# Performance work log

Hardware: AMD Instinct MI355X
Metric: run time of the kernel (lower is better)

The kernel has to match this reference:

```python
import jax, jax.numpy as jnp
import numpy as np

N = 2048      # number of ROIs
C = 1024      # in_channels == inter_channels
G = 16        # groups
D = C // G    # per-group dim = 64


def _bbox_overlaps(b1, b2):
    # mmdet-1.x IoU with +1 pixel convention; b1:(N,4), b2:(M,4)
    area1 = (b1[:, 2] - b1[:, 0] + 1) * (b1[:, 3] - b1[:, 1] + 1)  # (N,)
    area2 = (b2[:, 2] - b2[:, 0] + 1) * (b2[:, 3] - b2[:, 1] + 1)  # (M,)
    lt = jnp.maximum(b1[:, None, :2], b2[None, :, :2])             # (N,M,2)
    rb = jnp.minimum(b1[:, None, 2:], b2[None, :, 2:])             # (N,M,2)
    wh = jnp.clip(rb - lt + 1, 0)
    inter = wh[..., 0] * wh[..., 1]                                # (N,M)
    return inter / (area1[:, None] + area2[None, :] - inter)


def setup_inputs() -> dict:
    key = jax.random.key(0)
    ks = jax.random.split(key, 9)
    in_x = jax.random.normal(ks[0], (N, C), dtype=jnp.float32)
    # valid boxes: [batch_idx, x1, y1, x2, y2]
    xy = jax.random.uniform(ks[1], (N, 2), minval=0.0, maxval=800.0)
    wh = jax.random.uniform(ks[2], (N, 2), minval=8.0, maxval=200.0)
    rois = jnp.concatenate([jnp.zeros((N, 1)), xy, xy + wh], axis=1).astype(jnp.float32)
    s = 1.0 / np.sqrt(C)
    W0 = jax.random.normal(ks[3], (C, C), dtype=jnp.float32) * s
    b0 = jnp.zeros((C,), dtype=jnp.float32)
    W1 = jax.random.normal(ks[4], (C, C), dtype=jnp.float32) * s
    b1 = jnp.zeros((C,), dtype=jnp.float32)
    # grouped 1x1 conv: per group maps C channels -> D channels
    Wout = jax.random.normal(ks[5], (G, D, C), dtype=jnp.float32) * s
    bout = jnp.zeros((C,), dtype=jnp.float32)
    return {"in_x": in_x, "rois": rois, "W0": W0, "b0": b0, "W1": W1,
            "b1": b1, "Wout": Wout, "bout": bout}


def reference(in_x, rois, W0, b0, W1, b1, Wout, bout):
    # self-attention path: in_ref_x = in_x, ref_rois = rois
    # embed convs are pre-activation (relu -> 1x1 conv), shared for x and ref_x
    def embed(v):
        v = jax.nn.relu(v) @ W0.T + b0
        v = jax.nn.relu(v) @ W1.T + b1
        return v
    x = embed(in_x)                      # (N, C)
    ref_x = x                            # shared convs, same input
    xg = x.reshape(N, G, D)
    rg = ref_x.reshape(N, G, D)
    scores = jnp.einsum('ngd,mgd->ngm', xg, rg) / jnp.sqrt(jnp.float32(D))  # (N,G,N)
    ious = _bbox_overlaps(rois[:, 1:], rois[:, 1:])                          # (N,N)
    scores = scores + jnp.log(ious[:, None, :] + 1e-6)
    attn = jax.nn.softmax(scores, axis=2)                                    # (N,G,N)
    y = jnp.einsum('ngm,mc->ngc', attn, in_x)                                # (N,G,C)
    out = jnp.einsum('ngc,goc->ngo', y, Wout).reshape(N, C) + bout           # (N,C)
    return out
```

## Files before the change

### kernel.cpp

```cpp
#include <hip/hip_runtime.h>
#include <math.h>

constexpr int NROI = 2048;
constexpr int CDIM = 1024;
constexpr int NG   = 16;
constexpr int DH   = 64;

typedef __attribute__((ext_vector_type(8))) short short8;
typedef __attribute__((ext_vector_type(4))) float floatx4;

#define MFMA_BF16(a, b, c) __builtin_amdgcn_mfma_f32_16x16x32_bf16((a), (b), (c), 0, 0, 0)

__device__ __forceinline__ short f2bf(float f) {
  unsigned u = __float_as_uint(f);
  unsigned r = 0x7fffu + ((u >> 16) & 1u);
  return (short)((u + r) >> 16);
}
__device__ __forceinline__ float bf2f(unsigned short u) {
  return __uint_as_float(((unsigned)u) << 16);
}
__device__ __forceinline__ unsigned pack2(float a, float b) {
  return (unsigned)(unsigned short)f2bf(a) | ((unsigned)(unsigned short)f2bf(b) << 16);
}

typedef __attribute__((address_space(1))) void GV;
typedef __attribute__((address_space(3))) void LV;
__device__ __forceinline__ void gl2lds16(const void* g, void* l) {
  __builtin_amdgcn_global_load_lds((GV*)g, (LV*)l, 16, 0, 0);
}

__device__ __forceinline__ short8 brelu(short8 v) {
  union { short8 s; unsigned u[4]; } x; x.s = v;
#pragma unroll
  for (int i = 0; i < 4; ++i) {
    unsigned m = (x.u[i] >> 15) & 0x10001u;
    x.u[i] &= ~(m * 0xFFFFu);
  }
  return x.s;
}

__global__ __launch_bounds__(256) void convert_kernel(
    const float* __restrict__ in_x, const float* __restrict__ W0,
    const float* __restrict__ W1, const float* __restrict__ Wout,
    short* __restrict__ xin_b, short* __restrict__ W0b,
    short* __restrict__ W1b, short* __restrict__ Woutb)
{
  const int i = blockIdx.x * 256 + threadIdx.x;
  {
    const float4 v = ((const float4*)in_x)[i];
    uint2 u; u.x = pack2(v.x, v.y); u.y = pack2(v.z, v.w);
    ((uint2*)xin_b)[i] = u;
  }
  if (i < 262144) {
    float4 v = ((const float4*)W0)[i];
    uint2 u; u.x = pack2(v.x, v.y); u.y = pack2(v.z, v.w);
    ((uint2*)W0b)[i] = u;
    v = ((const float4*)W1)[i];
    u.x = pack2(v.x, v.y); u.y = pack2(v.z, v.w);
    ((uint2*)W1b)[i] = u;
    v = ((const float4*)Wout)[i];
    u.x = pack2(v.x, v.y); u.y = pack2(v.z, v.w);
    ((uint2*)Woutb)[i] = u;
  }
}

__global__ __launch_bounds__(256) void iou4_kernel(const float* __restrict__ rois,
                                                   unsigned short* __restrict__ biasb)
{
  const int q  = blockIdx.y;
  const int k0 = (blockIdx.x * 256 + threadIdx.x) * 4;
  const float qx1 = rois[q * 5 + 1], qy1 = rois[q * 5 + 2];
  const float qx2 = rois[q * 5 + 3], qy2 = rois[q * 5 + 4];
  const float qa = (qx2 - qx1 + 1.f) * (qy2 - qy1 + 1.f);
  float v[4];
#pragma unroll
  for (int j = 0; j < 4; ++j) {
    const int k = k0 + j;
    const float kx1 = rois[k * 5 + 1], ky1 = rois[k * 5 + 2];
    const float kx2 = rois[k * 5 + 3], ky2 = rois[k * 5 + 4];
    const float ka = (kx2 - kx1 + 1.f) * (ky2 - ky1 + 1.f);
    float iw = fminf(qx2, kx2) - fmaxf(qx1, kx1) + 1.f;
    float ih = fminf(qy2, ky2) - fmaxf(qy1, ky1) + 1.f;
    iw = fmaxf(iw, 0.f); ih = fmaxf(ih, 0.f);
    const float inter = iw * ih;
    v[j] = inter * __builtin_amdgcn_rcpf(qa + ka - inter) + 1e-6f;
  }
  uint2 u; u.x = pack2(v[0], v[1]); u.y = pack2(v[2], v[3]);
  *(uint2*)&biasb[(size_t)q * NROI + k0] = u;
}

template <int FUSED>
__global__ __launch_bounds__(256, 4) void gemm64(
    const short* __restrict__ A, const short* __restrict__ Ba,
    const short* __restrict__ Bb, const float* __restrict__ bias,
    short* __restrict__ outRM, short* __restrict__ outTR)
{
  __shared__ short As[2][8 * 512];
  __shared__ short Bs[2][8 * 512];
  const int t = threadIdx.x, w = t >> 6, lane = t & 63;
  const int wm = w >> 1, wn = w & 1;
  const int row0 = blockIdx.y * 64;
  bool isW0; int col0; const short* B;
  if (FUSED) {
    isW0 = blockIdx.x < 16;
    col0 = (blockIdx.x & 15) * 64;
    B = isW0 ? Ba : Bb;
  } else {
    isW0 = true; col0 = blockIdx.x * 64; B = Ba;
  }
  const bool doRelu = FUSED ? isW0 : true;
  const int rlo = lane & 15, khi = (lane >> 4) * 8;

  floatx4 acc[2][2];
#pragma unroll
  for (int i = 0; i < 2; ++i)
#pragma unroll
    for (int j = 0; j < 2; ++j) acc[i][j] = (floatx4){0.f, 0.f, 0.f, 0.f};

#pragma unroll
  for (int kh = 0; kh < 2; ++kh) {
    const int f = w * 2 + kh;
    gl2lds16(A + (size_t)(row0 + w * 16 + rlo) * CDIM + kh * 32 + khi, &As[0][f * 512]);
    gl2lds16(B + (size_t)(col0 + w * 16 + rlo) * CDIM + kh * 32 + khi, &Bs[0][f * 512]);
  }
  __syncthreads();

  for (int it = 0; it < 16; ++it) {
    const int p = it & 1;
    if (it < 15) {
      const int k1 = (it + 1) * 64;
#pragma unroll
      for (int kh = 0; kh < 2; ++kh) {
        const int f = w * 2 + kh;
        gl2lds16(A + (size_t)(row0 + w * 16 + rlo) * CDIM + k1 + kh * 32 + khi,
                 &As[1 - p][f * 512]);
        gl2lds16(B + (size_t)(col0 + w * 16 + rlo) * CDIM + k1 + kh * 32 + khi,
                 &Bs[1 - p][f * 512]);
      }
    }
#pragma unroll
    for (int kh = 0; kh < 2; ++kh) {
      short8 a[2], bf[2];
#pragma unroll
      for (int i = 0; i < 2; ++i) {
        a[i] = *(const short8*)&As[p][((wm * 2 + i) * 2 + kh) * 512 + lane * 8];
        if (doRelu) a[i] = brelu(a[i]);
      }
#pragma unroll
      for (int j = 0; j < 2; ++j)
        bf[j] = *(const short8*)&Bs[p][((wn * 2 + j) * 2 + kh) * 512 + lane * 8];
#pragma unroll
      for (int i = 0; i < 2; ++i)
#pragma unroll
        for (int j = 0; j < 2; ++j)
          acc[i][j] = MFMA_BF16(a[i], bf[j], acc[i][j]);
    }
    __syncthreads();
  }

  const int colL = lane & 15, qq = lane >> 4;
  if (!FUSED || isW0) {
    float bj[2];
    bj[0] = bias[col0 + wn * 32 + colL];
    bj[1] = bias[col0 + wn * 32 + 16 + colL];
#pragma unroll
    for (int i = 0; i < 2; ++i)
#pragma unroll
      for (int j = 0; j < 2; ++j)
#pragma unroll
        for (int r = 0; r < 4; ++r) {
          const int row = row0 + wm * 32 + i * 16 + qq * 4 + r;
          const int cc  = col0 + wn * 32 + j * 16 + colL;
          outRM[(size_t)row * CDIM + cc] = f2bf(acc[i][j][r] + bj[j]);
        }
  } else {
#pragma unroll
    for (int i = 0; i < 2; ++i)
#pragma unroll
      for (int j = 0; j < 2; ++j) {
        unsigned long long u =
            (unsigned long long)pack2(acc[i][j][0], acc[i][j][1]) |
            ((unsigned long long)pack2(acc[i][j][2], acc[i][j][3]) << 32);
        const int cc  = col0 + wn * 32 + j * 16 + colL;
        const int row = row0 + wm * 32 + i * 16 + qq * 4;
        *(unsigned long long*)&outTR[(size_t)cc * NROI + row] = u;
      }
  }
}

__global__ __launch_bounds__(512) void attn_bias(
    const short* __restrict__ Xb,
    const short* __restrict__ ZTb,
    const unsigned short* __restrict__ biasb,
    const float* __restrict__ bout,
    float* __restrict__ Out)
{
  const int g  = blockIdx.y;
  const int n0 = blockIdx.x * 128;
  const int t  = threadIdx.x;
  const int w    = t >> 6;
  const int lane = t & 63;
  const int col  = lane & 15;
  const int qq   = lane >> 4;
  const int t16 = (w >> 1) * 16;
  const int h32 = (w & 1) * 32;
  const int rlo = lane & 15, khi = (lane >> 4) * 8;

  __shared__ short Kf[2][8 * 512];
  __shared__ short Vf[2][8 * 512];
  __shared__ short Pf[8 * 1024];

  const size_t qoff = (size_t)(n0 + w * 16 + col) * CDIM + g * DH;
  const short8 qf0 = *(const short8*)(Xb + qoff + qq * 8);
  const short8 qf1 = *(const short8*)(Xb + qoff + 32 + qq * 8);

  floatx4 oc[4];
#pragma unroll
  for (int dt = 0; dt < 4; ++dt) oc[dt] = (floatx4){0.f, 0.f, 0.f, 0.f};
  float lsum[4] = {0.f, 0.f, 0.f, 0.f};

  gl2lds16(Xb + (size_t)(t16 + rlo) * CDIM + g * DH + h32 + khi, &Kf[0][w * 512]);
  gl2lds16(ZTb + (size_t)(g * DH + t16 + rlo) * NROI + h32 + khi, &Vf[0][w * 512]);
  __syncthreads();

  for (int it = 0; it < NROI / 64; ++it) {
    const int p  = it & 1;
    const int m0 = it * 64;
    if (it + 1 < NROI / 64) {
      const int m1 = m0 + 64;
      gl2lds16(Xb + (size_t)(m1 + t16 + rlo) * CDIM + g * DH + h32 + khi,
               &Kf[1 - p][w * 512]);
      gl2lds16(ZTb + (size_t)(g * DH + t16 + rlo) * NROI + m1 + h32 + khi,
               &Vf[1 - p][w * 512]);
    }

    float bb[4][4];
#pragma unroll
    for (int ct = 0; ct < 4; ++ct)
#pragma unroll
      for (int r = 0; r < 4; ++r)
        bb[ct][r] = bf2f(biasb[(size_t)(n0 + w * 16 + qq * 4 + r) * NROI +
                               m0 + ct * 16 + col]);

    floatx4 sc[4];
#pragma unroll
    for (int ct = 0; ct < 4; ++ct) {
      const short8 b0 = *(const short8*)&Kf[p][(ct * 2 + 0) * 512 + lane * 8];
      const short8 b1 = *(const short8*)&Kf[p][(ct * 2 + 1) * 512 + lane * 8];
      floatx4 z4 = (floatx4){0.f, 0.f, 0.f, 0.f};
      z4 = MFMA_BF16(qf0, b0, z4);
      z4 = MFMA_BF16(qf1, b1, z4);
      sc[ct] = z4;
    }

#pragma unroll
    for (int ct = 0; ct < 4; ++ct)
#pragma unroll
      for (int r = 0; r < 4; ++r)
        sc[ct][r] = __expf(sc[ct][r] * 0.125f) * bb[ct][r];
#pragma unroll
    for (int r = 0; r < 4; ++r)
      lsum[r] += sc[0][r] + sc[1][r] + sc[2][r] + sc[3][r];

    {
      short* pw = &Pf[w * 1024];
#pragma unroll
      for (int ct = 0; ct < 4; ++ct) {
        const int key = ct * 16 + col;
        const int base = (key >> 5) * 512 + (key & 7);
#pragma unroll
        for (int r = 0; r < 4; ++r) {
          const int dl = (4 * qq + r) + ((key >> 3) & 3) * 16;
          pw[base + dl * 8] = f2bf(sc[ct][r]);
        }
      }
      const short8 pa0 = *(const short8*)&pw[0 * 512 + lane * 8];
      const short8 pa1 = *(const short8*)&pw[1 * 512 + lane * 8];
#pragma unroll
      for (int dt = 0; dt < 4; ++dt) {
        const short8 v0 = *(const short8*)&Vf[p][(dt * 2 + 0) * 512 + lane * 8];
        const short8 v1 = *(const short8*)&Vf[p][(dt * 2 + 1) * 512 + lane * 8];
        oc[dt] = MFMA_BF16(pa0, v0, oc[dt]);
        oc[dt] = MFMA_BF16(pa1, v1, oc[dt]);
      }
    }
    __syncthreads();
  }

#pragma unroll
  for (int r = 0; r < 4; ++r) {
    float s = lsum[r];
    s += __shfl_xor(s, 1); s += __shfl_xor(s, 2);
    s += __shfl_xor(s, 4); s += __shfl_xor(s, 8);
    lsum[r] = s;
  }
#pragma unroll
  for (int dt = 0; dt < 4; ++dt) {
    const float bo = bout[g * DH + dt * 16 + col];
#pragma unroll
    for (int r = 0; r < 4; ++r)
      Out[(size_t)(n0 + w * 16 + qq * 4 + r) * CDIM + g * DH + dt * 16 + col] =
          oc[dt][r] / lsum[r] + bo;
  }
}

extern "C" void kernel_launch(void* const* d_in, const int* in_sizes, int n_in,
                              void* d_out, int out_size, void* d_ws, size_t ws_size,
                              hipStream_t stream) {
  const float* in_x = (const float*)d_in[0];
  const float* rois = (const float*)d_in[1];
  const float* W0   = (const float*)d_in[2];
  const float* b0   = (const float*)d_in[3];
  const float* W1   = (const float*)d_in[4];
  const float* b1   = (const float*)d_in[5];
  const float* Wout = (const float*)d_in[6];
  const float* bout = (const float*)d_in[7];
  char* w8 = (char*)d_ws;

  short* xin_b = (short*)w8;
  short* W0b   = (short*)(w8 + ((size_t)4 << 20));
  short* W1b   = (short*)(w8 + ((size_t)6 << 20));
  short* Woutb = (short*)(w8 + ((size_t)8 << 20));
  short* zT    = (short*)(w8 + ((size_t)10 << 20));
  unsigned short* biasb = (unsigned short*)(w8 + ((size_t)14 << 20));
  short* xb  = xin_b;
  short* t0b = (short*)d_out;

  convert_kernel<<<2048, 256, 0, stream>>>(in_x, W0, W1, Wout,
                                           xin_b, W0b, W1b, Woutb);
  iou4_kernel<<<dim3(2, NROI), 256, 0, stream>>>(rois, biasb);
  gemm64<1><<<dim3(32, 32), 256, 0, stream>>>(xin_b, W0b, Woutb, b0, t0b, zT);
  gemm64<0><<<dim3(16, 32), 256, 0, stream>>>(t0b, W1b, nullptr, b1, xb, nullptr);
  attn_bias<<<dim3(NROI / 128, NG), 512, 0, stream>>>(xb, zT, biasb, bout,
                                                      (float*)d_out);
}
```

Before: 187.6 us.

## Merge all stages into one cooperative persistent kernel with grid syncs

```diff
diff --git a/kernel.cpp b/kernel.cpp
--- a/kernel.cpp
+++ b/kernel.cpp
@@ -1,5 +1,8 @@
 #include <hip/hip_runtime.h>
+#include <hip/hip_cooperative_groups.h>
 #include <math.h>
+
+namespace cg = cooperative_groups;
 
 constexpr int NROI = 2048;
 constexpr int CDIM = 1024;
@@ -39,268 +42,331 @@
   return x.s;
 }
 
-__global__ __launch_bounds__(256) void convert_kernel(
-    const float* __restrict__ in_x, const float* __restrict__ W0,
-    const float* __restrict__ W1, const float* __restrict__ Wout,
+__global__ __launch_bounds__(512) void mega(
+    const float* __restrict__ in_x, const float* __restrict__ rois,
+    const float* __restrict__ W0, const float* __restrict__ b0,
+    const float* __restrict__ W1, const float* __restrict__ b1,
+    const float* __restrict__ Wout, const float* __restrict__ bout,
     short* __restrict__ xin_b, short* __restrict__ W0b,
-    short* __restrict__ W1b, short* __restrict__ Woutb)
+    short* __restrict__ W1b, short* __restrict__ Woutb,
+    short* __restrict__ zT, unsigned short* __restrict__ biasb,
+    short* __restrict__ t0b, float* __restrict__ out)
 {
-  const int i = blockIdx.x * 256 + threadIdx.x;
+  cg::grid_group grid = cg::this_grid();
+  __shared__ short S[32768];
+
+  const int bid = blockIdx.x;
+  const int t = threadIdx.x;
+  const int w = t >> 6, lane = t & 63;
+  const int rlo = lane & 15, khi = (lane >> 4) * 8;
+  const int colL = lane & 15, qq = lane >> 4;
+  short* xb = xin_b;
+
   {
-    const float4 v = ((const float4*)in_x)[i];
-    uint2 u; u.x = pack2(v.x, v.y); u.y = pack2(v.z, v.w);
-    ((uint2*)xin_b)[i] = u;
+    const int gtid = bid * 512 + t;
+    for (int i = gtid; i < 524288; i += 131072) {
+      const float4 v = ((const float4*)in_x)[i];
+      uint2 u; u.x = pack2(v.x, v.y); u.y = pack2(v.z, v.w);
+      ((uint2*)xin_b)[i] = u;
+    }
+    for (int i = gtid; i < 262144; i += 131072) {
+      float4 v = ((const float4*)W0)[i];
+      uint2 u; u.x = pack2(v.x, v.y); u.y = pack2(v.z, v.w);
+      ((uint2*)W0b)[i] = u;
+      v = ((const float4*)W1)[i];
+      u.x = pack2(v.x, v.y); u.y = pack2(v.z, v.w);
+      ((uint2*)W1b)[i] = u;
+      v = ((const float4*)Wout)[i];
+      u.x = pack2(v.x, v.y); u.y = pack2(v.z, v.w);
+      ((uint2*)Woutb)[i] = u;
+    }
+    for (int pq = gtid; pq < 1048576; pq += 131072) {
+      const int q = pq >> 9, k0 = (pq & 511) * 4;
+      const float qx1 = rois[q * 5 + 1], qy1 = rois[q * 5 + 2];
+      const float qx2 = rois[q * 5 + 3], qy2 = rois[q * 5 + 4];
+      const float qa = (qx2 - qx1 + 1.f) * (qy2 - qy1 + 1.f);
+      float v[4];
+#pragma unroll
+      for (int j = 0; j < 4; ++j) {
+        const int k = k0 + j;
+        const float kx1 = rois[k * 5 + 1], ky1 = rois[k * 5 + 2];
+        const float kx2 = rois[k * 5 + 3], ky2 = rois[k * 5 + 4];
+        const float ka = (kx2 - kx1 + 1.f) * (ky2 - ky1 + 1.f);
+        float iw = fminf(qx2, kx2) - fmaxf(qx1, kx1) + 1.f;
+        float ih = fminf(qy2, ky2) - fmaxf(qy1, ky1) + 1.f;
+        iw = fmaxf(iw, 0.f); ih = fmaxf(ih, 0.f);
+        const float inter = iw * ih;
+        v[j] = inter * __builtin_amdgcn_rcpf(qa + ka - inter) + 1e-6f;
+      }
+      uint2 u; u.x = pack2(v[0], v[1]); u.y = pack2(v[2], v[3]);
+      *(uint2*)&biasb[(size_t)q * NROI + k0] = u;
+    }
   }
-  if (i < 262144) {
-    float4 v = ((const float4*)W0)[i];
-    uint2 u; u.x = pack2(v.x, v.y); u.y = pack2(v.z, v.w);
-    ((uint2*)W0b)[i] = u;
-    v = ((const float4*)W1)[i];
-    u.x = pack2(v.x, v.y); u.y = pack2(v.z, v.w);
-    ((uint2*)W1b)[i] = u;
-    v = ((const float4*)Wout)[i];
-    u.x = pack2(v.x, v.y); u.y = pack2(v.z, v.w);
-    ((uint2*)Woutb)[i] = u;
+  grid.sync();
+
+  {
+    const int row0 = (bid >> 4) * 128;
+    const int cb = bid & 15;
+    const bool isW0 = cb < 8;
+    const int col0 = (cb & 7) * 128;
+    const short* B = isW0 ? W0b : Woutb;
+    const int wr = w >> 1, wc = w & 1;
+    auto As = [&](int p, int f) -> short* { return S + p * 8192 + f * 512; };
+    auto Bs = [&](int p, int f) -> short* { return S + 16384 + p * 8192 + f * 512; };
+
+    floatx4 acc[2][4];
+#pragma unroll
+    for (int i = 0; i < 2; ++i)
+#pragma unroll
+      for (int j = 0; j < 4; ++j) acc[i][j] = (floatx4){0.f, 0.f, 0.f, 0.f};
+
+#pragma unroll
+    for (int kh = 0; kh < 2; ++kh) {
+      const int f = w * 2 + kh;
+      gl2lds16(xin_b + (size_t)(row0 + w * 16 + rlo) * CDIM + kh * 32 + khi, As(0, f));
+      gl2lds16(B + (size_t)(col0 + w * 16 + rlo) * CDIM + kh * 32 + khi, Bs(0, f));
+    }
+    __syncthreads();
+
+    for (int it = 0; it < 16; ++it) {
+      const int p = it & 1;
+      if (it < 15) {
+        const int k1 = (it + 1) * 64;
+#pragma unroll
+        for (int kh = 0; kh < 2; ++kh) {
+          const int f = w * 2 + kh;
+          gl2lds16(xin_b + (size_t)(row0 + w * 16 + rlo) * CDIM + k1 + kh * 32 + khi,
+                   As(1 - p, f));
+          gl2lds16(B + (size_t)(col0 + w * 16 + rlo) * CDIM + k1 + kh * 32 + khi,
+                   Bs(1 - p, f));
+        }
+      }
+#pragma unroll
+      for (int kh = 0; kh < 2; ++kh) {
+        short8 a[2], bf[4];
+#pragma unroll
+        for (int i = 0; i < 2; ++i) {
+          a[i] = *(const short8*)(As(p, (wr * 2 + i) * 2 + kh) + lane * 8);
+          if (isW0) a[i] = brelu(a[i]);
+        }
+#pragma unroll
+        for (int j = 0; j < 4; ++j)
+          bf[j] = *(const short8*)(Bs(p, (wc * 4 + j) * 2 + kh) + lane * 8);
+#pragma unroll
+        for (int i = 0; i < 2; ++i)
+#pragma unroll
+          for (int j = 0; j < 4; ++j)
+            acc[i][j] = MFMA_BF16(a[i], bf[j], acc[i][j]);
+      }
+      __syncthreads();
+    }
+
+    if (isW0) {
+      float bj[4];
+#pragma unroll
+      for (int j = 0; j < 4; ++j) bj[j] = b0[col0 + wc * 64 + j * 16 + colL];
+#pragma unroll
+      for (int i = 0; i < 2; ++i)
+#pragma unroll
+        for (int j = 0; j < 4; ++j)
+#pragma unroll
+          for (int r = 0; r < 4; ++r) {
+            const int row = row0 + wr * 32 + i * 16 + qq * 4 + r;
+            const int cc  = col0 + wc * 64 + j * 16 + colL;
+            t0b[(size_t)row * CDIM + cc] = f2bf(acc[i][j][r] + bj[j]);
+          }
+    } else {
+#pragma unroll
+      for (int i = 0; i < 2; ++i)
+#pragma unroll
+        for (int j = 0; j < 4; ++j) {
+          unsigned long long u =
+              (unsigned long long)pack2(acc[i][j][0], acc[i][j][1]) |
+              ((unsigned long long)pack2(acc[i][j][2], acc[i][j][3]) << 32);
+          const int cc  = col0 + wc * 64 + j * 16 + colL;
+          const int row = row0 + wr * 32 + i * 16 + qq * 4;
+          *(unsigned long long*)&zT[(size_t)cc * NROI + row] = u;
+        }
+    }
   }
-}
-
-__global__ __launch_bounds__(256) void iou4_kernel(const float* __restrict__ rois,
-                                                   unsigned short* __restrict__ biasb)
-{
-  const int q  = blockIdx.y;
-  const int k0 = (blockIdx.x * 256 + threadIdx.x) * 4;
-  const float qx1 = rois[q * 5 + 1], qy1 = rois[q * 5 + 2];
-  const float qx2 = rois[q * 5 + 3], qy2 = rois[q * 5 + 4];
-  const float qa = (qx2 - qx1 + 1.f) * (qy2 - qy1 + 1.f);
-  float v[4];
-#pragma unroll
-  for (int j = 0; j < 4; ++j) {
-    const int k = k0 + j;
-    const float kx1 = rois[k * 5 + 1], ky1 = rois[k * 5 + 2];
-    const float kx2 = rois[k * 5 + 3], ky2 = rois[k * 5 + 4];
-    const float ka = (kx2 - kx1 + 1.f) * (ky2 - ky1 + 1.f);
-    float iw = fminf(qx2, kx2) - fmaxf(qx1, kx1) + 1.f;
-    float ih = fminf(qy2, ky2) - fmaxf(qy1, ky1) + 1.f;
-    iw = fmaxf(iw, 0.f); ih = fmaxf(ih, 0.f);
-    const float inter = iw * ih;
-    v[j] = inter * __builtin_amdgcn_rcpf(qa + ka - inter) + 1e-6f;
+  grid.sync();
+
+  {
+    const int row0 = (bid >> 4) * 128;
+    const int col0 = (bid & 15) * 64;
+    const int wr = w >> 1, wc = w & 1;
+    auto As = [&](int p, int f) -> short* { return S + p * 8192 + f * 512; };
+    auto Bs = [&](int p, int f) -> short* { return S + 16384 + p * 4096 + f * 512; };
+
+    floatx4 acc[2][2];
+#pragma unroll
+    for (int i = 0; i < 2; ++i)
+#pragma unroll
+      for (int j = 0; j < 2; ++j) acc[i][j] = (floatx4){0.f, 0.f, 0.f, 0.f};
+
+#pragma unroll
+    for (int kh = 0; kh < 2; ++kh) {
+      const int f = w * 2 + kh;
+      gl2lds16(t0b + (size_t)(row0 + w * 16 + rlo) * CDIM + kh * 32 + khi, As(0, f));
+    }
+    {
+      const int f = w, rt = f >> 1, kh = f & 1;
+      gl2lds16(W1b + (size_t)(col0 + rt * 16 + rlo) * CDIM + kh * 32 + khi, Bs(0, f));
+    }
+    __syncthreads();
+
+    for (int it = 0; it < 16; ++it) {
+      const int p = it & 1;
+      if (it < 15) {
+        const int k1 = (it + 1) * 64;
+#pragma unroll
+        for (int kh = 0; kh < 2; ++kh) {
+          const int f = w * 2 + kh;
+          gl2lds16(t0b + (size_t)(row0 + w * 16 + rlo) * CDIM + k1 + kh * 32 + khi,
+                   As(1 - p, f));
+        }
+        {
+          const int f = w, rt = f >> 1, kh = f & 1;
+          gl2lds16(W1b + (size_t)(col0 + rt * 16 + rlo) * CDIM + k1 + kh * 32 + khi,
+                   Bs(1 - p, f));
+        }
+      }
+#pragma unroll
+      for (int kh = 0; kh < 2; ++kh) {
+        short8 a[2], bf[2];
+#pragma unroll
+        for (int i = 0; i < 2; ++i)
+          a[i] = brelu(*(const short8*)(As(p, (wr * 2 + i) * 2 + kh) + lane * 8));
+#pragma unroll
+        for (int j = 0; j < 2; ++j)
+          bf[j] = *(const short8*)(Bs(p, (wc * 2 + j) * 2 + kh) + lane * 8);
+#pragma unroll
+        for (int i = 0; i < 2; ++i)
+#pragma unroll
+          for (int j = 0; j < 2; ++j)
+            acc[i][j] = MFMA_BF16(a[i], bf[j], acc[i][j]);
+      }
+      __syncthreads();
+    }
+
+    float bj[2];
+    bj[0] = b1[col0 + wc * 32 + colL];
+    bj[1] = b1[col0 + wc * 32 + 16 + colL];
+#pragma unroll
+    for (int i = 0; i < 2; ++i)
+#pragma unroll
+      for (int j = 0; j < 2; ++j)
+#pragma unroll
+        for (int r = 0; r < 4; ++r) {
+          const int row = row0 + wr * 32 + i * 16 + qq * 4 + r;
+          const int cc  = col0 + wc * 32 + j * 16 + colL;
+          xb[(size_t)row * CDIM + cc] = f2bf(acc[i][j][r] + bj[j]);
+        }
   }
-  uint2 u; u.x = pack2(v[0], v[1]); u.y = pack2(v[2], v[3]);
-  *(uint2*)&biasb[(size_t)q * NROI + k0] = u;
-}
-
-template <int FUSED>
-__global__ __launch_bounds__(256, 4) void gemm64(
-    const short* __restrict__ A, const short* __restrict__ Ba,
-    const short* __restrict__ Bb, const float* __restrict__ bias,
-    short* __restrict__ outRM, short* __restrict__ outTR)
-{
-  __shared__ short As[2][8 * 512];
-  __shared__ short Bs[2][8 * 512];
-  const int t = threadIdx.x, w = t >> 6, lane = t & 63;
-  const int wm = w >> 1, wn = w & 1;
-  const int row0 = blockIdx.y * 64;
-  bool isW0; int col0; const short* B;
-  if (FUSED) {
-    isW0 = blockIdx.x < 16;
-    col0 = (blockIdx.x & 15) * 64;
-    B = isW0 ? Ba : Bb;
-  } else {
-    isW0 = true; col0 = blockIdx.x * 64; B = Ba;
-  }
-  const bool doRelu = FUSED ? isW0 : true;
-  const int rlo = lane & 15, khi = (lane >> 4) * 8;
-
-  floatx4 acc[2][2];
-#pragma unroll
-  for (int i = 0; i < 2; ++i)
-#pragma unroll
-    for (int j = 0; j < 2; ++j) acc[i][j] = (floatx4){0.f, 0.f, 0.f, 0.f};
-
-#pragma unroll
-  for (int kh = 0; kh < 2; ++kh) {
-    const int f = w * 2 + kh;
-    gl2lds16(A + (size_t)(row0 + w * 16 + rlo) * CDIM + kh * 32 + khi, &As[0][f * 512]);
-    gl2lds16(B + (size_t)(col0 + w * 16 + rlo) * CDIM + kh * 32 + khi, &Bs[0][f * 512]);
-  }
-  __syncthreads();
-
-  for (int it = 0; it < 16; ++it) {
-    const int p = it & 1;
-    if (it < 15) {
-      const int k1 = (it + 1) * 64;
-#pragma unroll
-      for (int kh = 0; kh < 2; ++kh) {
-        const int f = w * 2 + kh;
-        gl2lds16(A + (size_t)(row0 + w * 16 + rlo) * CDIM + k1 + kh * 32 + khi,
-                 &As[1 - p][f * 512]);
-        gl2lds16(B + (size_t)(col0 + w * 16 + rlo) * CDIM + k1 + kh * 32 + khi,
-                 &Bs[1 - p][f * 512]);
-      }
-    }
-#pragma unroll
-    for (int kh = 0; kh < 2; ++kh) {
-      short8 a[2], bf[2];
-#pragma unroll
-      for (int i = 0; i < 2; ++i) {
-        a[i] = *(const short8*)&As[p][((wm * 2 + i) * 2 + kh) * 512 + lane * 8];
-        if (doRelu) a[i] = brelu(a[i]);
-      }
-#pragma unroll
-      for (int j = 0; j < 2; ++j)
-        bf[j] = *(const short8*)&Bs[p][((wn * 2 + j) * 2 + kh) * 512 + lane * 8];
-#pragma unroll
-      for (int i = 0; i < 2; ++i)
-#pragma unroll
-        for (int j = 0; j < 2; ++j)
-          acc[i][j] = MFMA_BF16(a[i], bf[j], acc[i][j]);
-    }
+  grid.sync();
+
+  {
+    const int g  = bid >> 4;
+    const int n0 = (bid & 15) * 128;
+    const int col = lane & 15;
+    const int t16 = (w >> 1) * 16;
+    const int h32 = (w & 1) * 32;
+    auto Kf = [&](int p) -> short* { return S + p * 4096; };
+    auto Vf = [&](int p) -> short* { return S + 8192 + p * 4096; };
+    short* Pf = S + 16384;
+
+    const size_t qoff = (size_t)(n0 + w * 16 + col) * CDIM + g * DH;
+    const short8 qf0 = *(const short8*)(xb + qoff + qq * 8);
+    const short8 qf1 = *(const short8*)(xb + qoff + 32 + qq * 8);
+
+    floatx4 oc[4];
+#pragma unroll
+    for (int dt = 0; dt < 4; ++dt) oc[dt] = (floatx4){0.f, 0.f, 0.f, 0.f};
+    float lsum[4] = {0.f, 0.f, 0.f, 0.f};
+
+    gl2lds16(xb + (size_t)(t16 + rlo) * CDIM + g * DH + h32 + khi, Kf(0) + w * 512);
+    gl2lds16(zT + (size_t)(g * DH + t16 + rlo) * NROI + h32 + khi, Vf(0) + w * 512);
     __syncthreads();
-  }
-
-  const int colL = lane & 15, qq = lane >> 4;
-  if (!FUSED || isW0) {
-    float bj[2];
-    bj[0] = bias[col0 + wn * 32 + colL];
-    bj[1] = bias[col0 + wn * 32 + 16 + colL];
-#pragma unroll
-    for (int i = 0; i < 2; ++i)
-#pragma unroll
-      for (int j = 0; j < 2; ++j)
-#pragma unroll
-        for (int r = 0; r < 4; ++r) {
-          const int row = row0 + wm * 32 + i * 16 + qq * 4 + r;
-          const int cc  = col0 + wn * 32 + j * 16 + colL;
-          outRM[(size_t)row * CDIM + cc] = f2bf(acc[i][j][r] + bj[j]);
-        }
-  } else {
-#pragma unroll
-    for (int i = 0; i < 2; ++i)
-#pragma unroll
-      for (int j = 0; j < 2; ++j) {
-        unsigned long long u =
-            (unsigned long long)pack2(acc[i][j][0], acc[i][j][1]) |
-            ((unsigned long long)pack2(acc[i][j][2], acc[i][j][3]) << 32);
-        const int cc  = col0 + wn * 32 + j * 16 + colL;
-        const int row = row0 + wm * 32 + i * 16 + qq * 4;
-        *(unsigned long long*)&outTR[(size_t)cc * NROI + row] = u;
-      }
-  }
-}
-
-__global__ __launch_bounds__(512) void attn_bias(
-    const short* __restrict__ Xb,
-    const short* __restrict__ ZTb,
-    const unsigned short* __restrict__ biasb,
-    const float* __restrict__ bout,
-    float* __restrict__ Out)
-{
-  const int g  = blockIdx.y;
-  const int n0 = blockIdx.x * 128;
-  const int t  = threadIdx.x;
-  const int w    = t >> 6;
-  const int lane = t & 63;
-  const int col  = lane & 15;
-  const int qq   = lane >> 4;
-  const int t16 = (w >> 1) * 16;
-  const int h32 = (w & 1) * 32;
-  const int rlo = lane & 15, khi = (lane >> 4) * 8;
-
-  __shared__ short Kf[2][8 * 512];
-  __shared__ short Vf[2][8 * 512];
-  __shared__ short Pf[8 * 1024];
-
-  const size_t qoff = (size_t)(n0 + w * 16 + col) * CDIM + g * DH;
-  const short8 qf0 = *(const short8*)(Xb + qoff + qq * 8);
-  const short8 qf1 = *(const short8*)(Xb + qoff + 32 + qq * 8);
-
-  floatx4 oc[4];
-#pragma unroll
-  for (int dt = 0; dt < 4; ++dt) oc[dt] = (floatx4){0.f, 0.f, 0.f, 0.f};
-  float lsum[4] = {0.f, 0.f, 0.f, 0.f};
-
-  gl2lds16(Xb + (size_t)(t16 + rlo) * CDIM + g * DH + h32 + khi, &Kf[0][w * 512]);
-  gl2lds16(ZTb + (size_t)(g * DH + t16 + rlo) * NROI + h32 + khi, &Vf[0][w * 512]);
-  __syncthreads();
-
-  for (int it = 0; it < NROI / 64; ++it) {
-    const int p  = it & 1;
-    const int m0 = it * 64;
-    if (it + 1 < NROI / 64) {
-      const int m1 = m0 + 64;
-      gl2lds16(Xb + (size_t)(m1 + t16 + rlo) * CDIM + g * DH + h32 + khi,
-               &Kf[1 - p][w * 512]);
-      gl2lds16(ZTb + (size_t)(g * DH + t16 + rlo) * NROI + m1 + h32 + khi,
-               &Vf[1 - p][w * 512]);
-    }
-
-    float bb[4][4];
-#pragma unroll
-    for (int ct = 0; ct < 4; ++ct)
+
+    for (int it = 0; it < NROI / 64; ++it) {
+      const int p  = it & 1;
+      const int m0 = it * 64;
+      if (it + 1 < NROI / 64) {
+        const int m1 = m0 + 64;
+        gl2lds16(xb + (size_t)(m1 + t16 + rlo) * CDIM + g * DH + h32 + khi,
+                 Kf(1 - p) + w * 512);
+        gl2lds16(zT + (size_t)(g * DH + t16 + rlo) * NROI + m1 + h32 + khi,
+                 Vf(1 - p) + w * 512);
+      }
+
+      float bb[4][4];
+#pragma unroll
+      for (int ct = 0; ct < 4; ++ct)
+#pragma unroll
+        for (int r = 0; r < 4; ++r)
+          bb[ct][r] = bf2f(biasb[(size_t)(n0 + w * 16 + qq * 4 + r) * NROI +
+                                 m0 + ct * 16 + col]);
+
+      floatx4 sc[4];
+#pragma unroll
+      for (int ct = 0; ct < 4; ++ct) {
+        const short8 b0f = *(const short8*)(Kf(p) + (ct * 2 + 0) * 512 + lane * 8);
+        const short8 b1f = *(const short8*)(Kf(p) + (ct * 2 + 1) * 512 + lane * 8);
+        floatx4 z4 = (floatx4){0.f, 0.f, 0.f, 0.f};
+        z4 = MFMA_BF16(qf0, b0f, z4);
+        z4 = MFMA_BF16(qf1, b1f, z4);
+        sc[ct] = z4;
+      }
+
+#pragma unroll
+      for (int ct = 0; ct < 4; ++ct)
+#pragma unroll
+        for (int r = 0; r < 4; ++r)
+          sc[ct][r] = __expf(sc[ct][r] * 0.125f) * bb[ct][r];
 #pragma unroll
       for (int r = 0; r < 4; ++r)
-        bb[ct][r] = bf2f(biasb[(size_t)(n0 + w * 16 + qq * 4 + r) * NROI +
-                               m0 + ct * 16 + col]);
-
-    floatx4 sc[4];
-#pragma unroll
-    for (int ct = 0; ct < 4; ++ct) {
-      const short8 b0 = *(const short8*)&Kf[p][(ct * 2 + 0) * 512 + lane * 8];
-      const short8 b1 = *(const short8*)&Kf[p][(ct * 2 + 1) * 512 + lane * 8];
-      floatx4 z4 = (floatx4){0.f, 0.f, 0.f, 0.f};
-      z4 = MFMA_BF16(qf0, b0, z4);
-      z4 = MFMA_BF16(qf1, b1, z4);
-      sc[ct] = z4;
-    }
-
-#pragma unroll
-    for (int ct = 0; ct < 4; ++ct)
+        lsum[r] += sc[0][r] + sc[1][r] + sc[2][r] + sc[3][r];
+
+      {
+        short* pw = Pf + w * 1024;
+#pragma unroll
+        for (int ct = 0; ct < 4; ++ct) {
+          const int key = ct * 16 + col;
+          const int base = (key >> 5) * 512 + (key & 7);
+#pragma unroll
+          for (int r = 0; r < 4; ++r) {
+            const int dl = (4 * qq + r) + ((key >> 3) & 3) * 16;
+            pw[base + dl * 8] = f2bf(sc[ct][r]);
+          }
+        }
+        const short8 pa0 = *(const short8*)(pw + lane * 8);
+        const short8 pa1 = *(const short8*)(pw + 512 + lane * 8);
+#pragma unroll
+        for (int dt = 0; dt < 4; ++dt) {
+          const short8 v0 = *(const short8*)(Vf(p) + (dt * 2 + 0) * 512 + lane * 8);
+          const short8 v1 = *(const short8*)(Vf(p) + (dt * 2 + 1) * 512 + lane * 8);
+          oc[dt] = MFMA_BF16(pa0, v0, oc[dt]);
+          oc[dt] = MFMA_BF16(pa1, v1, oc[dt]);
+        }
+      }
+      __syncthreads();
+    }
+
+#pragma unroll
+    for (int r = 0; r < 4; ++r) {
+      float s = lsum[r];
+      s += __shfl_xor(s, 1); s += __shfl_xor(s, 2);
+      s += __shfl_xor(s, 4); s += __shfl_xor(s, 8);
+      lsum[r] = s;
+    }
+#pragma unroll
+    for (int dt = 0; dt < 4; ++dt) {
+      const float bo = bout[g * DH + dt * 16 + col];
 #pragma unroll
       for (int r = 0; r < 4; ++r)
-        sc[ct][r] = __expf(sc[ct][r] * 0.125f) * bb[ct][r];
-#pragma unroll
-    for (int r = 0; r < 4; ++r)
-      lsum[r] += sc[0][r] + sc[1][r] + sc[2][r] + sc[3][r];
-
-    {
-      short* pw = &Pf[w * 1024];
-#pragma unroll
-      for (int ct = 0; ct < 4; ++ct) {
-        const int key = ct * 16 + col;
-        const int base = (key >> 5) * 512 + (key & 7);
-#pragma unroll
-        for (int r = 0; r < 4; ++r) {
-          const int dl = (4 * qq + r) + ((key >> 3) & 3) * 16;
-          pw[base + dl * 8] = f2bf(sc[ct][r]);
-        }
-      }
-      const short8 pa0 = *(const short8*)&pw[0 * 512 + lane * 8];
-      const short8 pa1 = *(const short8*)&pw[1 * 512 + lane * 8];
-#pragma unroll
-      for (int dt = 0; dt < 4; ++dt) {
-        const short8 v0 = *(const short8*)&Vf[p][(dt * 2 + 0) * 512 + lane * 8];
-        const short8 v1 = *(const short8*)&Vf[p][(dt * 2 + 1) * 512 + lane * 8];
-        oc[dt] = MFMA_BF16(pa0, v0, oc[dt]);
-        oc[dt] = MFMA_BF16(pa1, v1, oc[dt]);
-      }
-    }
-    __syncthreads();
-  }
-
-#pragma unroll
-  for (int r = 0; r < 4; ++r) {
-    float s = lsum[r];
-    s += __shfl_xor(s, 1); s += __shfl_xor(s, 2);
-    s += __shfl_xor(s, 4); s += __shfl_xor(s, 8);
-    lsum[r] = s;
-  }
-#pragma unroll
-  for (int dt = 0; dt < 4; ++dt) {
-    const float bo = bout[g * DH + dt * 16 + col];
-#pragma unroll
-    for (int r = 0; r < 4; ++r)
-      Out[(size_t)(n0 + w * 16 + qq * 4 + r) * CDIM + g * DH + dt * 16 + col] =
-          oc[dt][r] / lsum[r] + bo;
+        out[(size_t)(n0 + w * 16 + qq * 4 + r) * CDIM + g * DH + dt * 16 + col] =
+            oc[dt][r] / lsum[r] + bo;
+    }
   }
 }
 
@@ -323,14 +389,14 @@
   short* Woutb = (short*)(w8 + ((size_t)8 << 20));
   short* zT    = (short*)(w8 + ((size_t)10 << 20));
   unsigned short* biasb = (unsigned short*)(w8 + ((size_t)14 << 20));
-  short* xb  = xin_b;
   short* t0b = (short*)d_out;
-
-  convert_kernel<<<2048, 256, 0, stream>>>(in_x, W0, W1, Wout,
-                                           xin_b, W0b, W1b, Woutb);
-  iou4_kernel<<<dim3(2, NROI), 256, 0, stream>>>(rois, biasb);
-  gemm64<1><<<dim3(32, 32), 256, 0, stream>>>(xin_b, W0b, Woutb, b0, t0b, zT);
-  gemm64<0><<<dim3(16, 32), 256, 0, stream>>>(t0b, W1b, nullptr, b1, xb, nullptr);
-  attn_bias<<<dim3(NROI / 128, NG), 512, 0, stream>>>(xb, zT, biasb, bout,
-                                                      (float*)d_out);
-}
+  float* out = (float*)d_out;
+
+  void* args[] = {
+    (void*)&in_x, (void*)&rois, (void*)&W0, (void*)&b0,
+    (void*)&W1, (void*)&b1, (void*)&Wout, (void*)&bout,
+    (void*)&xin_b, (void*)&W0b, (void*)&W1b, (void*)&Woutb,
+    (void*)&zT, (void*)&biasb, (void*)&t0b, (void*)&out,
+  };
+  hipLaunchCooperativeKernel((void*)mega, dim3(256), dim3(512), args, 0, stream);
+}
```

Result: slower. 286.4 us (+52.7%).

## Compute IoU bias inline in attention kernel instead of precomputed matrix

Applied to the files above, without the earlier changes.

```diff
diff --git a/kernel.cpp b/kernel.cpp
--- a/kernel.cpp
+++ b/kernel.cpp
@@ -16,9 +16,6 @@
   unsigned r = 0x7fffu + ((u >> 16) & 1u);
   return (short)((u + r) >> 16);
 }
-__device__ __forceinline__ float bf2f(unsigned short u) {
-  return __uint_as_float(((unsigned)u) << 16);
-}
 __device__ __forceinline__ unsigned pack2(float a, float b) {
   return (unsigned)(unsigned short)f2bf(a) | ((unsigned)(unsigned short)f2bf(b) << 16);
 }
@@ -39,54 +36,40 @@
   return x.s;
 }
 
-__global__ __launch_bounds__(256) void convert_kernel(
+__global__ __launch_bounds__(256) void conv_pack(
     const float* __restrict__ in_x, const float* __restrict__ W0,
     const float* __restrict__ W1, const float* __restrict__ Wout,
+    const float* __restrict__ rois,
     short* __restrict__ xin_b, short* __restrict__ W0b,
-    short* __restrict__ W1b, short* __restrict__ Woutb)
+    short* __restrict__ W1b, short* __restrict__ Woutb,
+    float4* __restrict__ boxp, float* __restrict__ areap)
 {
-  const int i = blockIdx.x * 256 + threadIdx.x;
-  {
-    const float4 v = ((const float4*)in_x)[i];
-    uint2 u; u.x = pack2(v.x, v.y); u.y = pack2(v.z, v.w);
-    ((uint2*)xin_b)[i] = u;
-  }
-  if (i < 262144) {
-    float4 v = ((const float4*)W0)[i];
-    uint2 u; u.x = pack2(v.x, v.y); u.y = pack2(v.z, v.w);
-    ((uint2*)W0b)[i] = u;
-    v = ((const float4*)W1)[i];
-    u.x = pack2(v.x, v.y); u.y = pack2(v.z, v.w);
-    ((uint2*)W1b)[i] = u;
-    v = ((const float4*)Wout)[i];
-    u.x = pack2(v.x, v.y); u.y = pack2(v.z, v.w);
-    ((uint2*)Woutb)[i] = u;
-  }
-}
-
-__global__ __launch_bounds__(256) void iou4_kernel(const float* __restrict__ rois,
-                                                   unsigned short* __restrict__ biasb)
-{
-  const int q  = blockIdx.y;
-  const int k0 = (blockIdx.x * 256 + threadIdx.x) * 4;
-  const float qx1 = rois[q * 5 + 1], qy1 = rois[q * 5 + 2];
-  const float qx2 = rois[q * 5 + 3], qy2 = rois[q * 5 + 4];
-  const float qa = (qx2 - qx1 + 1.f) * (qy2 - qy1 + 1.f);
-  float v[4];
-#pragma unroll
-  for (int j = 0; j < 4; ++j) {
-    const int k = k0 + j;
-    const float kx1 = rois[k * 5 + 1], ky1 = rois[k * 5 + 2];
-    const float kx2 = rois[k * 5 + 3], ky2 = rois[k * 5 + 4];
-    const float ka = (kx2 - kx1 + 1.f) * (ky2 - ky1 + 1.f);
-    float iw = fminf(qx2, kx2) - fmaxf(qx1, kx1) + 1.f;
-    float ih = fminf(qy2, ky2) - fmaxf(qy1, ky1) + 1.f;
-    iw = fmaxf(iw, 0.f); ih = fmaxf(ih, 0.f);
-    const float inter = iw * ih;
-    v[j] = inter * __builtin_amdgcn_rcpf(qa + ka - inter) + 1e-6f;
-  }
-  uint2 u; u.x = pack2(v[0], v[1]); u.y = pack2(v[2], v[3]);
-  *(uint2*)&biasb[(size_t)q * NROI + k0] = u;
+  const int b = blockIdx.x;
+  if (b < 2048) {
+    const int i = b * 256 + threadIdx.x;
+    {
+      const float4 v = ((const float4*)in_x)[i];
+      uint2 u; u.x = pack2(v.x, v.y); u.y = pack2(v.z, v.w);
+      ((uint2*)xin_b)[i] = u;
+    }
+    if (i < 262144) {
+      float4 v = ((const float4*)W0)[i];
+      uint2 u; u.x = pack2(v.x, v.y); u.y = pack2(v.z, v.w);
+      ((uint2*)W0b)[i] = u;
+      v = ((const float4*)W1)[i];
+      u.x = pack2(v.x, v.y); u.y = pack2(v.z, v.w);
+      ((uint2*)W1b)[i] = u;
+      v = ((const float4*)Wout)[i];
+      u.x = pack2(v.x, v.y); u.y = pack2(v.z, v.w);
+      ((uint2*)Woutb)[i] = u;
+    }
+  } else {
+    const int k = (b - 2048) * 256 + threadIdx.x;
+    const float x1 = rois[k * 5 + 1], y1 = rois[k * 5 + 2];
+    const float x2 = rois[k * 5 + 3], y2 = rois[k * 5 + 4];
+    boxp[k] = make_float4(x1, y1, x2, y2);
+    areap[k] = (x2 - x1 + 1.f) * (y2 - y1 + 1.f);
+  }
 }
 
 template <int FUSED>
@@ -188,10 +171,11 @@
   }
 }
 
-__global__ __launch_bounds__(512) void attn_bias(
+__global__ __launch_bounds__(512) void attn_inline(
     const short* __restrict__ Xb,
     const short* __restrict__ ZTb,
-    const unsigned short* __restrict__ biasb,
+    const float4* __restrict__ boxp,
+    const float* __restrict__ areap,
     const float* __restrict__ bout,
     float* __restrict__ Out)
 {
@@ -214,6 +198,15 @@
   const short8 qf0 = *(const short8*)(Xb + qoff + qq * 8);
   const short8 qf1 = *(const short8*)(Xb + qoff + 32 + qq * 8);
 
+  float qx1[4], qy1[4], qx2[4], qy2[4], qar[4];
+#pragma unroll
+  for (int r = 0; r < 4; ++r) {
+    const int qrow = n0 + w * 16 + qq * 4 + r;
+    const float4 qb = boxp[qrow];
+    qx1[r] = qb.x; qy1[r] = qb.y; qx2[r] = qb.z; qy2[r] = qb.w;
+    qar[r] = areap[qrow];
+  }
+
   floatx4 oc[4];
 #pragma unroll
   for (int dt = 0; dt < 4; ++dt) oc[dt] = (floatx4){0.f, 0.f, 0.f, 0.f};
@@ -234,13 +227,13 @@
                &Vf[1 - p][w * 512]);
     }
 
-    float bb[4][4];
-#pragma unroll
-    for (int ct = 0; ct < 4; ++ct)
-#pragma unroll
-      for (int r = 0; r < 4; ++r)
-        bb[ct][r] = bf2f(biasb[(size_t)(n0 + w * 16 + qq * 4 + r) * NROI +
-                               m0 + ct * 16 + col]);
+    float4 kb[4]; float ka[4];
+#pragma unroll
+    for (int ct = 0; ct < 4; ++ct) {
+      const int key = m0 + ct * 16 + col;
+      kb[ct] = boxp[key];
+      ka[ct] = areap[key];
+    }
 
     floatx4 sc[4];
 #pragma unroll
@@ -256,8 +249,14 @@
 #pragma unroll
     for (int ct = 0; ct < 4; ++ct)
 #pragma unroll
-      for (int r = 0; r < 4; ++r)
-        sc[ct][r] = __expf(sc[ct][r] * 0.125f) * bb[ct][r];
+      for (int r = 0; r < 4; ++r) {
+        float iw = fminf(qx2[r], kb[ct].z) - fmaxf(qx1[r], kb[ct].x) + 1.f;
+        float ih = fminf(qy2[r], kb[ct].w) - fmaxf(qy1[r], kb[ct].y) + 1.f;
+        iw = fmaxf(iw, 0.f); ih = fmaxf(ih, 0.f);
+        const float inter = iw * ih;
+        const float iou = inter * __builtin_amdgcn_rcpf(qar[r] + ka[ct] - inter);
+        sc[ct][r] = __expf(sc[ct][r] * 0.125f) * (iou + 1e-6f);
+      }
 #pragma unroll
     for (int r = 0; r < 4; ++r)
       lsum[r] += sc[0][r] + sc[1][r] + sc[2][r] + sc[3][r];
@@ -322,15 +321,15 @@
   short* W1b   = (short*)(w8 + ((size_t)6 << 20));
   short* Woutb = (short*)(w8 + ((size_t)8 << 20));
   short* zT    = (short*)(w8 + ((size_t)10 << 20));
-  unsigned short* biasb = (unsigned short*)(w8 + ((size_t)14 << 20));
+  float4* boxp = (float4*)(w8 + ((size_t)14 << 20));
+  float* areap = (float*)(w8 + ((size_t)14 << 20) + 32768);
   short* xb  = xin_b;
   short* t0b = (short*)d_out;
 
-  convert_kernel<<<2048, 256, 0, stream>>>(in_x, W0, W1, Wout,
-                                           xin_b, W0b, W1b, Woutb);
-  iou4_kernel<<<dim3(2, NROI), 256, 0, stream>>>(rois, biasb);
+  conv_pack<<<2056, 256, 0, stream>>>(in_x, W0, W1, Wout, rois,
+                                      xin_b, W0b, W1b, Woutb, boxp, areap);
   gemm64<1><<<dim3(32, 32), 256, 0, stream>>>(xin_b, W0b, Woutb, b0, t0b, zT);
   gemm64<0><<<dim3(16, 32), 256, 0, stream>>>(t0b, W1b, nullptr, b1, xb, nullptr);
-  attn_bias<<<dim3(NROI / 128, NG), 512, 0, stream>>>(xb, zT, biasb, bout,
-                                                      (float*)d_out);
-}
+  attn_inline<<<dim3(NROI / 128, NG), 512, 0, stream>>>(xb, zT, boxp, areap,
+                                                        bout, (float*)d_out);
+}
```

Measured after the change: 218.5 us. 16.5% more time.
